# Performance work log

Measured on AMD Instinct MI355X. Metric: run time of the kernel, lower is better.

Reference implementation:

```python
import jax, jax.numpy as jnp
import numpy as np

P = 0.9  # CLOP swap probability (init kwarg)


def _index_permute(key, n_element, dim):
    """Faithful port of CLOPLayer._index_permute: sequential conditional
    neighbor swaps over a flat index array, expressed as a lax.scan.
    Swap choices r in {0..4} with probs (1-p/2, p/8, p/8, p/8, p/8);
    r maps to offset {0, +1, -1, +dim, -dim}; swap only if r!=0 and
    0 < idx < n_element (strict >0, matching the original code)."""
    probs = jnp.array([1.0 - P / 2, P / 8, P / 8, P / 8, P / 8], dtype=jnp.float32)
    # loop runs i over abs(range(-n+1, n)) -> 2n-1 steps
    iters = jnp.abs(jnp.arange(-n_element + 1, n_element, dtype=jnp.int32))
    rs = jax.random.choice(key, 5, shape=(iters.shape[0],), p=probs)
    offsets = jnp.array([0, 1, -1, dim, -dim], dtype=jnp.int32)

    def step(perm, inp):
        i, r = inp
        idx = i + offsets[r]
        do = (r != 0) & (idx > 0) & (idx < n_element)
        idx_c = jnp.clip(idx, 0, n_element - 1)
        a = perm[i]
        b = perm[idx_c]
        # conditional swap; when do is False both writes restore originals
        perm = perm.at[i].set(jnp.where(do, b, a))
        perm = perm.at[idx_c].set(jnp.where(do, a, b))
        return perm, None

    perm0 = jnp.arange(n_element, dtype=jnp.int32)
    perm, _ = jax.lax.scan(step, perm0, (iters, rs))
    return perm


def setup_inputs() -> dict:
    key = jax.random.key(0)
    x = jax.random.normal(key, (512, 9, 84, 84), dtype=jnp.float32)
    return {"x": x}


def reference(x):
    B, C, H, W = x.shape
    n = H * W  # n_element of x[0,0]; dim = int(sqrt(n)) == H for square images
    perm = _index_permute(jax.random.key(42), n, H)
    flat = x.reshape(B, C, n)
    # torch.gather(flat, 2, idx) with idx broadcast over (B, C)
    res = jnp.take(flat, perm, axis=2)
    return res.reshape(x.shape)
```

## Files before the change

### kernel.cpp

```cpp
#include <hip/hip_runtime.h>

#define N_ELEM   7056
#define DIM      84
#define M_STEPS  14111
#define N_ROWS   4608
#define NCHUNK   96
#define KSTEPS   147
#define WINW     320
#define TPB      256

__device__ __forceinline__ void threefry2x32(unsigned k0, unsigned k1,
                                             unsigned x0, unsigned x1,
                                             unsigned &o0, unsigned &o1) {
  const unsigned ks0 = k0, ks1 = k1, ks2 = k0 ^ k1 ^ 0x1BD11BDAu;
  x0 += ks0; x1 += ks1;
#define ROTL(x, r) (((x) << (r)) | ((x) >> (32 - (r))))
#define RND(r) { x0 += x1; x1 = ROTL(x1, r); x1 ^= x0; }
  RND(13) RND(15) RND(26) RND(6)
  x0 += ks1; x1 += ks2 + 1u;
  RND(17) RND(29) RND(16) RND(24)
  x0 += ks2; x1 += ks0 + 2u;
  RND(13) RND(15) RND(26) RND(6)
  x0 += ks0; x1 += ks1 + 3u;
  RND(17) RND(29) RND(16) RND(24)
  x0 += ks1; x1 += ks2 + 4u;
  RND(13) RND(15) RND(26) RND(6)
  x0 += ks2; x1 += ks0 + 5u;
  o0 = x0; o1 = x1;
#undef RND
#undef ROTL
}

__device__ __forceinline__ int r_from_bits(unsigned bits) {
  const float p8 = 0.1125f;
  const float q0 = 0.55f;
  const float q1 = q0 + p8;
  const float q2 = q1 + p8;
  const float q3 = q2 + p8;
  const float q4 = q3 + p8;
  float u  = __uint_as_float((bits >> 9) | 0x3F800000u) - 1.0f;
  float rv = q4 * (1.0f - u);
  return (int)(q0 < rv) + (int)(q1 < rv) + (int)(q2 < rv) + (int)(q3 < rv);
}

__device__ __forceinline__ void chunk_bounds(int c, int &t0, int &t1, int &lo, int &hi) {
  t0 = c * KSTEPS;
  t1 = t0 + KSTEPS; if (t1 > M_STEPS) t1 = M_STEPS;
  int a0 = t0 - (N_ELEM - 1);       if (a0 < 0) a0 = -a0;
  int a1 = (t1 - 1) - (N_ELEM - 1); if (a1 < 0) a1 = -a1;
  int imax = a0 > a1 ? a0 : a1;
  int imin;
  if (t0 <= N_ELEM - 1 && t1 - 1 >= N_ELEM - 1) imin = 0;
  else imin = a0 < a1 ? a0 : a1;
  lo = imin - DIM; if (lo < 0) lo = 0;
  hi = imax + DIM; if (hi > N_ELEM - 1) hi = N_ELEM - 1;
}

__global__ __launch_bounds__(TPB) void chunk_kernel(unsigned* __restrict__ winG) {
  __shared__ __align__(16) unsigned short w[WINW];
  __shared__ unsigned char rs[KSTEPS + 1];

  const int c = blockIdx.x, tid = threadIdx.x;
  int t0, t1, lo, hi; chunk_bounds(c, t0, t1, lo, hi);
  const int nt = t1 - t0;

  for (int e = tid; e < WINW; e += TPB) w[e] = (unsigned short)(lo + e);
  if (tid < nt) {
    unsigned y0, y1;
    threefry2x32(0u, 42u, 0u, (unsigned)(t0 + tid), y0, y1);
    rs[tid] = (unsigned char)r_from_bits(y0 ^ y1);
  }
  __syncthreads();

  if (tid == 0) {
    for (int k = 0; k < nt; ++k) {
      int t = t0 + k;
      int i = t - (N_ELEM - 1); if (i < 0) i = -i;
      int r = rs[k];
      int off = (r == 1) ? 1 : (r == 2) ? -1 : (r == 3) ? DIM : (r == 4) ? -DIM : 0;
      int idx = i + off;
      bool doit = (r != 0) && (idx > 0) && (idx < N_ELEM);
      int je = doit ? idx : i;
      unsigned short a = w[i  - lo];
      unsigned short b = w[je - lo];
      w[i  - lo] = b;
      w[je - lo] = a;
    }
  }
  __syncthreads();

  const unsigned* ws32 = (const unsigned*)w;
  if (tid < WINW / 2) winG[c * (WINW / 2) + tid] = ws32[tid];
}

#define TRACE_BLOCKS 28
__global__ __launch_bounds__(TPB) void trace_kernel(const unsigned* __restrict__ winG,
                                                    int* __restrict__ permG) {
  __shared__ __align__(16) unsigned short w[NCHUNK * WINW];
  const int tid = threadIdx.x;

  uint4* w4 = (uint4*)w;
  const uint4* g4 = (const uint4*)winG;
  const int n4 = (NCHUNK * WINW * 2) / 16;
  for (int k = tid; k < n4; k += TPB) w4[k] = g4[k];
  __syncthreads();

  if (tid < 252) {
    int y = blockIdx.x * 252 + tid;
    for (int c = NCHUNK - 1; c >= 0; --c) {
      int t0, t1, lo, hi; chunk_bounds(c, t0, t1, lo, hi);
      unsigned e = (unsigned)(y - lo);
      if (e <= (unsigned)(hi - lo)) y = (int)w[c * WINW + e];
    }
    permG[blockIdx.x * 252 + tid] = y;
  }
}

#define GROWS 16
#define NJV   (N_ELEM / 4)
__global__ __launch_bounds__(TPB) void gather_kernel(const float* __restrict__ x,
                                                     const int* __restrict__ perm,
                                                     float* __restrict__ out) {
  int jv = blockIdx.x * TPB + threadIdx.x;
  bool valid = (jv < NJV);
  int4 p = valid ? ((const int4*)perm)[jv] : make_int4(0, 0, 0, 0);
  int r0 = blockIdx.y * GROWS;
  const float* xb = x   + (size_t)r0 * N_ELEM;
  float*       ob = out + (size_t)r0 * N_ELEM;
#pragma unroll
  for (int rr = 0; rr < GROWS; ++rr) {
    const float* xr = xb + (size_t)rr * N_ELEM;
    float4 v;
    v.x = xr[p.x]; v.y = xr[p.y]; v.z = xr[p.z]; v.w = xr[p.w];
    if (valid) ((float4*)(ob + (size_t)rr * N_ELEM))[jv] = v;
  }
}

extern "C" void kernel_launch(void* const* d_in, const int* in_sizes, int n_in,
                              void* d_out, int out_size, void* d_ws, size_t ws_size,
                              hipStream_t stream) {
  const float* x = (const float*)d_in[0];
  float* out = (float*)d_out;

  unsigned* winG = (unsigned*)d_ws;
  int* perm = (int*)((char*)d_ws + NCHUNK * WINW * 2);

  chunk_kernel<<<NCHUNK, TPB, 0, stream>>>(winG);
  trace_kernel<<<TRACE_BLOCKS, TPB, 0, stream>>>(winG, perm);

  dim3 grid((NJV + TPB - 1) / TPB, N_ROWS / GROWS);
  gather_kernel<<<grid, TPB, 0, stream>>>(x, perm, out);
}
```

Before: 275.4 us.

## Shorten serial swap chunks and gather each row through shared memory

The permutation build is split into 384 smaller chunks of 37 steps, so each block's serial single-thread swap loop is about four times shorter. The trace kernel now streams the windows through shared memory in passes of 128 chunks. The gather kernel now gives each row its own block: the row is loaded into LDS with coalesced float4 reads and permuted from there, replacing scattered global loads. The cost is more chunk windows for the trace to walk and one block per row with a 28 KB LDS footprint, which limits occupancy.

```diff
diff --git a/kernel.cpp b/kernel.cpp
--- a/kernel.cpp
+++ b/kernel.cpp
@@ -4,10 +4,11 @@
 #define DIM      84
 #define M_STEPS  14111
 #define N_ROWS   4608
-#define NCHUNK   96
-#define KSTEPS   147
-#define WINW     320
+#define NCHUNK   384
+#define KSTEPS   37
+#define WINW     208
 #define TPB      256
+#define NJV      1764
 
 __device__ __forceinline__ void threefry2x32(unsigned k0, unsigned k1,
                                              unsigned x0, unsigned x1,
@@ -44,7 +45,7 @@
 }
 
 __device__ __forceinline__ void chunk_bounds(int c, int &t0, int &t1, int &lo, int &hi) {
-  t0 = c * KSTEPS;
+  t0 = c * KSTEPS; if (t0 > M_STEPS) t0 = M_STEPS;
   t1 = t0 + KSTEPS; if (t1 > M_STEPS) t1 = M_STEPS;
   int a0 = t0 - (N_ELEM - 1);       if (a0 < 0) a0 = -a0;
   int a1 = (t1 - 1) - (N_ELEM - 1); if (a1 < 0) a1 = -a1;
@@ -58,13 +59,13 @@
 
 __global__ __launch_bounds__(TPB) void chunk_kernel(unsigned* __restrict__ winG) {
   __shared__ __align__(16) unsigned short w[WINW];
-  __shared__ unsigned char rs[KSTEPS + 1];
+  __shared__ unsigned char rs[KSTEPS + 3];
 
   const int c = blockIdx.x, tid = threadIdx.x;
   int t0, t1, lo, hi; chunk_bounds(c, t0, t1, lo, hi);
   const int nt = t1 - t0;
 
-  for (int e = tid; e < WINW; e += TPB) w[e] = (unsigned short)(lo + e);
+  if (tid < WINW) w[tid] = (unsigned short)(lo + tid);
   if (tid < nt) {
     unsigned y0, y1;
     threefry2x32(0u, 42u, 0u, (unsigned)(t0 + tid), y0, y1);
@@ -89,50 +90,59 @@
   }
   __syncthreads();
 
-  const unsigned* ws32 = (const unsigned*)w;
-  if (tid < WINW / 2) winG[c * (WINW / 2) + tid] = ws32[tid];
+  const uint4* w4 = (const uint4*)w;
+  if (tid < WINW * 2 / 16) ((uint4*)winG)[c * (WINW * 2 / 16) + tid] = w4[tid];
 }
 
 #define TRACE_BLOCKS 28
+#define WPP 128
 __global__ __launch_bounds__(TPB) void trace_kernel(const unsigned* __restrict__ winG,
                                                     int* __restrict__ permG) {
-  __shared__ __align__(16) unsigned short w[NCHUNK * WINW];
+  __shared__ __align__(16) unsigned short w[WPP * WINW];
   const int tid = threadIdx.x;
+  const int U4_PER_WIN = WINW * 2 / 16;
 
-  uint4* w4 = (uint4*)w;
-  const uint4* g4 = (const uint4*)winG;
-  const int n4 = (NCHUNK * WINW * 2) / 16;
-  for (int k = tid; k < n4; k += TPB) w4[k] = g4[k];
-  __syncthreads();
+  int y = blockIdx.x * 252 + tid;
 
-  if (tid < 252) {
-    int y = blockIdx.x * 252 + tid;
-    for (int c = NCHUNK - 1; c >= 0; --c) {
-      int t0, t1, lo, hi; chunk_bounds(c, t0, t1, lo, hi);
-      unsigned e = (unsigned)(y - lo);
-      if (e <= (unsigned)(hi - lo)) y = (int)w[c * WINW + e];
+  for (int pass = NCHUNK / WPP - 1; pass >= 0; --pass) {
+    const int cbase = pass * WPP;
+    uint4* w4 = (uint4*)w;
+    const uint4* g4 = (const uint4*)winG + cbase * U4_PER_WIN;
+    for (int k = tid; k < WPP * U4_PER_WIN; k += TPB) w4[k] = g4[k];
+    __syncthreads();
+
+    if (tid < 252) {
+      for (int c = WPP - 1; c >= 0; --c) {
+        int t0, t1, lo, hi; chunk_bounds(cbase + c, t0, t1, lo, hi);
+        unsigned e = (unsigned)(y - lo);
+        if (e <= (unsigned)(hi - lo)) y = (int)w[c * WINW + e];
+      }
     }
-    permG[blockIdx.x * 252 + tid] = y;
+    __syncthreads();
   }
+
+  if (tid < 252) permG[blockIdx.x * 252 + tid] = y;
 }
 
-#define GROWS 16
-#define NJV   (N_ELEM / 4)
 __global__ __launch_bounds__(TPB) void gather_kernel(const float* __restrict__ x,
                                                      const int* __restrict__ perm,
                                                      float* __restrict__ out) {
-  int jv = blockIdx.x * TPB + threadIdx.x;
-  bool valid = (jv < NJV);
-  int4 p = valid ? ((const int4*)perm)[jv] : make_int4(0, 0, 0, 0);
-  int r0 = blockIdx.y * GROWS;
-  const float* xb = x   + (size_t)r0 * N_ELEM;
-  float*       ob = out + (size_t)r0 * N_ELEM;
-#pragma unroll
-  for (int rr = 0; rr < GROWS; ++rr) {
-    const float* xr = xb + (size_t)rr * N_ELEM;
-    float4 v;
-    v.x = xr[p.x]; v.y = xr[p.y]; v.z = xr[p.z]; v.w = xr[p.w];
-    if (valid) ((float4*)(ob + (size_t)rr * N_ELEM))[jv] = v;
+  __shared__ __align__(16) float row[N_ELEM];
+  const int r = blockIdx.x;
+  const int tid = threadIdx.x;
+
+  const float4* xr4 = (const float4*)(x + (size_t)r * N_ELEM);
+  float4* row4 = (float4*)row;
+  for (int v = tid; v < NJV; v += TPB) row4[v] = xr4[v];
+  __syncthreads();
+
+  float4* or4 = (float4*)(out + (size_t)r * N_ELEM);
+  const int4* p4 = (const int4*)perm;
+  for (int v = tid; v < NJV; v += TPB) {
+    int4 p = p4[v];
+    float4 o;
+    o.x = row[p.x]; o.y = row[p.y]; o.z = row[p.z]; o.w = row[p.w];
+    or4[v] = o;
   }
 }
 
@@ -147,7 +157,5 @@
 
   chunk_kernel<<<NCHUNK, TPB, 0, stream>>>(winG);
   trace_kernel<<<TRACE_BLOCKS, TPB, 0, stream>>>(winG, perm);
-
-  dim3 grid((NJV + TPB - 1) / TPB, N_ROWS / GROWS);
-  gather_kernel<<<grid, TPB, 0, stream>>>(x, perm, out);
+  gather_kernel<<<N_ROWS, TPB, 0, stream>>>(x, perm, out);
 }
```

Result: faster. 268.0 us (-2.7%).
